# Performance work log

Hardware: AMD Instinct MI355X
Metric: run time of the kernel (lower is better)

The kernel has to match this reference:

```python
import jax, jax.numpy as jnp
import numpy as np

TEMPERATURE = 0.07
NEG_INF = -1e9


def setup_inputs() -> dict:
    key = jax.random.key(0)
    k1, k2, k3, k4, k5 = jax.random.split(key, 5)
    B, L, H = 64, 256, 64
    query_embs = jax.random.normal(k1, (B, L, H), dtype=jnp.float32)
    key_embs = jax.random.normal(k2, (B, L, H), dtype=jnp.float32)
    labels = jax.random.randint(k3, (B,), 0, 2, dtype=jnp.int64)
    q_mask = jax.random.randint(k4, (B, L), 0, 2, dtype=jnp.int32)
    k_mask = jax.random.randint(k5, (B, L), 0, 2, dtype=jnp.int32)
    return {"query_embs": query_embs, "key_embs": key_embs, "labels": labels,
            "q_mask": q_mask, "k_mask": k_mask}


def reference(query_embs, key_embs, labels, q_mask, k_mask):
    # ColBERT-style late interaction over all B x B pairs.
    # sim: (B_q, B_k, Lq, Lk) token-level dot products.
    sim = jnp.einsum('bqh,ckh->bcqk', query_embs, key_embs)
    # Mask out padded key tokens before the max over key positions.
    sim = jnp.where(k_mask[None, :, None, :].astype(bool), sim, NEG_INF)
    maxsim = jnp.max(sim, axis=-1)                      # (B_q, B_k, Lq)
    qm = q_mask[:, None, :].astype(maxsim.dtype)        # (B_q, 1, Lq)
    scores = jnp.sum(maxsim * qm, axis=-1) / TEMPERATURE  # (B_q, B_k)
    # Cross-entropy on rows with labels==1, target = diagonal index.
    logp = jax.nn.log_softmax(scores, axis=-1)
    B = scores.shape[0]
    diag = logp[jnp.arange(B), jnp.arange(B)]           # (B,)
    w = labels.astype(scores.dtype)
    denom = jnp.maximum(jnp.sum(w), 1.0)
    return -jnp.sum(w * diag) / denom
```

## Files before the change

### kernel.cpp

```cpp
#include <hip/hip_runtime.h>
#include <math.h>

#define PB 64
#define PL 256
#define PH 64
#define TEMP 0.07f
#define NEG_INF_F (-1e9f)

#define KFTILE 1024
#define KFSLAB (16 * KFTILE)
#define BGRP   2

typedef short short8 __attribute__((ext_vector_type(8)));
typedef float f32x4 __attribute__((ext_vector_type(4)));

__device__ __forceinline__ unsigned short f32_to_bf16(float f) {
    unsigned int u = __float_as_uint(f);
    u += 0x7FFFu + ((u >> 16) & 1u);
    return (unsigned short)(u >> 16);
}

__device__ __forceinline__ int frag_off(int p, int cc) {
    return ((p >> 4) * KFTILE) + ((cc >> 3) * 512) +
           (((((cc >> 1) & 3) * 16) + (p & 15)) * 8) + ((cc & 1) * 4);
}

__global__ __launch_bounds__(256)
void prep_kernel(const float* __restrict__ Q,
                 const float* __restrict__ K,
                 const int*   __restrict__ kmask,
                 const int*   __restrict__ qmask,
                 unsigned short* __restrict__ Qfrag,
                 unsigned short* __restrict__ Kfrag,
                 int* __restrict__ nvK,
                 int* __restrict__ nvQ) {
    const int tid  = threadIdx.x;
    const int lane = tid & 63;
    const int wave = tid >> 6;
    __shared__ int posArr[PL];
    __shared__ int wcnt[4];

    const bool isQ = (blockIdx.x >= 256);
    const int  bid = isQ ? (blockIdx.x - 256) : blockIdx.x;
    const int  idx     = bid >> 2;
    const int  quarter = bid & 3;

    const int* mask = isQ ? (qmask + idx * PL) : (kmask + idx * PL);
    const int km = mask[tid];
    unsigned long long bal = __ballot(km != 0);
    int within = __popcll(bal & ((1ull << lane) - 1ull));
    if (lane == 0) wcnt[wave] = __popcll(bal);
    __syncthreads();
    int base = 0;
    #pragma unroll
    for (int w = 0; w < 4; ++w) base += (w < wave) ? wcnt[w] : 0;
    posArr[tid] = km ? (base + within) : -1;
    const int nv = wcnt[0] + wcnt[1] + wcnt[2] + wcnt[3];
    __syncthreads();

    const int sub = lane >> 4;
    const int cl  = lane & 15;
    const float* src = (isQ ? Q : K) + (size_t)idx * PL * PH;
    unsigned short* slab = (isQ ? Qfrag : Kfrag) + (size_t)idx * KFSLAB;

    #pragma unroll
    for (int it = 0; it < 4; ++it) {
        int r = quarter * 64 + it * 16 + wave * 4 + sub;
        int p = posArr[r];
        if (p >= 0) {
            float4 v = *(const float4*)(src + (size_t)r * PH + cl * 4);
            ushort4 o;
            o.x = f32_to_bf16(v.x); o.y = f32_to_bf16(v.y);
            o.z = f32_to_bf16(v.z); o.w = f32_to_bf16(v.w);
            *(ushort4*)(slab + frag_off(p, cl)) = o;
        }
    }

    if (!isQ) {
        const int rows16 = (nv + 15) & ~15;
        const int padChunks = (rows16 - nv) * 16;
        if (tid < padChunks) {
            int row = nv + (tid >> 4);
            if (row >= quarter * 64 && row < quarter * 64 + 64)
                *(ushort4*)(slab + frag_off(row, tid & 15)) = (ushort4){0, 0, 0, 0};
        }
        if (quarter == 0 && tid == 0) nvK[idx] = nv;
    } else {
        #pragma unroll
        for (int it = 0; it < 4; ++it) {
            int id2 = it * 256 + tid;
            int row = quarter * 64 + (id2 >> 4);
            if (row >= nv)
                *(ushort4*)(slab + frag_off(row, id2 & 15)) = (ushort4){0, 0, 0, 0};
        }
        if (quarter == 0 && tid == 0) nvQ[idx] = nv;
    }
}

__global__ __launch_bounds__(256, 2)
void colbert_scores_mfma(const unsigned short* __restrict__ Qfrag,
                         const unsigned short* __restrict__ Kfrag,
                         const int*   __restrict__ nvK,
                         const int*   __restrict__ nvQ,
                         float*       __restrict__ scores) {
    const int c  = blockIdx.x;
    const int bg = blockIdx.y;
    const int tid  = threadIdx.x;
    const int wave = tid >> 6;
    const int lane = tid & 63;
    const int n    = lane & 15;

    __shared__ float red[BGRP][4];

    const int nv       = nvK[c];
    const int ntFull   = nv >> 4;
    const int tailCols = nv & 15;

    const int b0  = bg * BGRP;
    const int nq0 = nvQ[b0];
    const int nq1 = nvQ[b0 + 1];
    const int ntQP = ((nq0 > nq1 ? nq0 : nq1) + 31) >> 5;

    const f32x4 ZERO4 = (f32x4){0.f, 0.f, 0.f, 0.f};
    const float biasv = (n < tailCols) ? 0.0f : NEG_INF_F;
    const f32x4 BIAS4 = (f32x4){biasv, biasv, biasv, biasv};

    const unsigned short* kb = Kfrag + (size_t)c * KFSLAB + lane * 8;

    float partial[BGRP] = {0.0f, 0.0f};

    for (int qp = wave; qp < ntQP; qp += 4) {
        short8 aA[BGRP][2][2];
        #pragma unroll
        for (int bi = 0; bi < BGRP; ++bi) {
            const unsigned short* qbase = Qfrag + (size_t)(b0 + bi) * KFSLAB
                                         + qp * 2 * KFTILE + lane * 8;
            aA[bi][0][0] = *(const short8*)(qbase);
            aA[bi][0][1] = *(const short8*)(qbase + 512);
            aA[bi][1][0] = *(const short8*)(qbase + 1024);
            aA[bi][1][1] = *(const short8*)(qbase + 1536);
        }

        float maxv[BGRP][2][4];
        #pragma unroll
        for (int bi = 0; bi < BGRP; ++bi)
            #pragma unroll
            for (int t = 0; t < 2; ++t)
                #pragma unroll
                for (int r = 0; r < 4; ++r) maxv[bi][t][r] = NEG_INF_F;

        int ct = 0;
        for (; ct + 1 < ntFull; ct += 2) {
            const unsigned short* ka = kb + ct * KFTILE;
            short8 kA0 = *(const short8*)(ka);
            short8 kA1 = *(const short8*)(ka + 512);
            short8 kB0 = *(const short8*)(ka + 1024);
            short8 kB1 = *(const short8*)(ka + 1536);

            #pragma unroll
            for (int bi = 0; bi < BGRP; ++bi)
                #pragma unroll
                for (int t = 0; t < 2; ++t) {
                    f32x4 accA = __builtin_amdgcn_mfma_f32_16x16x32_bf16(aA[bi][t][0], kA0, ZERO4, 0, 0, 0);
                    accA = __builtin_amdgcn_mfma_f32_16x16x32_bf16(aA[bi][t][1], kA1, accA, 0, 0, 0);
                    f32x4 accB = __builtin_amdgcn_mfma_f32_16x16x32_bf16(aA[bi][t][0], kB0, ZERO4, 0, 0, 0);
                    accB = __builtin_amdgcn_mfma_f32_16x16x32_bf16(aA[bi][t][1], kB1, accB, 0, 0, 0);
                    #pragma unroll
                    for (int r = 0; r < 4; ++r)
                        maxv[bi][t][r] = fmaxf(maxv[bi][t][r], fmaxf(accA[r], accB[r]));
                }
        }

        if (ntFull & 1) {
            const unsigned short* ka = kb + ct * KFTILE;
            short8 k0 = *(const short8*)(ka);
            short8 k1 = *(const short8*)(ka + 512);
            #pragma unroll
            for (int bi = 0; bi < BGRP; ++bi)
                #pragma unroll
                for (int t = 0; t < 2; ++t) {
                    f32x4 acc = __builtin_amdgcn_mfma_f32_16x16x32_bf16(aA[bi][t][0], k0, ZERO4, 0, 0, 0);
                    acc = __builtin_amdgcn_mfma_f32_16x16x32_bf16(aA[bi][t][1], k1, acc, 0, 0, 0);
                    #pragma unroll
                    for (int r = 0; r < 4; ++r)
                        maxv[bi][t][r] = fmaxf(maxv[bi][t][r], acc[r]);
                }
            ct++;
        }

        if (tailCols) {
            const unsigned short* ka = kb + ct * KFTILE;
            short8 k0 = *(const short8*)(ka);
            short8 k1 = *(const short8*)(ka + 512);
            #pragma unroll
            for (int bi = 0; bi < BGRP; ++bi)
                #pragma unroll
                for (int t = 0; t < 2; ++t) {
                    f32x4 acc = __builtin_amdgcn_mfma_f32_16x16x32_bf16(aA[bi][t][0], k0, BIAS4, 0, 0, 0);
                    acc = __builtin_amdgcn_mfma_f32_16x16x32_bf16(aA[bi][t][1], k1, acc, 0, 0, 0);
                    #pragma unroll
                    for (int r = 0; r < 4; ++r)
                        maxv[bi][t][r] = fmaxf(maxv[bi][t][r], acc[r]);
                }
        }

        #pragma unroll
        for (int bi = 0; bi < BGRP; ++bi)
            #pragma unroll
            for (int t = 0; t < 2; ++t)
                #pragma unroll
                for (int r = 0; r < 4; ++r) {
                    float mv = maxv[bi][t][r];
                    mv = fmaxf(mv, __shfl_xor(mv, 1, 16));
                    mv = fmaxf(mv, __shfl_xor(mv, 2, 16));
                    mv = fmaxf(mv, __shfl_xor(mv, 4, 16));
                    mv = fmaxf(mv, __shfl_xor(mv, 8, 16));
                    if (n == 0) partial[bi] += mv;
                }
    }

    #pragma unroll
    for (int bi = 0; bi < BGRP; ++bi) {
        float p = partial[bi];
        p += __shfl_xor(p, 16, 64);
        p += __shfl_xor(p, 32, 64);
        if (lane == 0) red[bi][wave] = p;
    }

    __syncthreads();
    if (tid < BGRP) {
        float total = red[tid][0] + red[tid][1] + red[tid][2] + red[tid][3];
        scores[(b0 + tid) * PB + c] = total * (1.0f / TEMP);
    }
}

__global__ void finalize_kernel(const float* __restrict__ scores,
                                const int*   __restrict__ labels,
                                float*       __restrict__ out) {
    const int r = threadIdx.x;
    const float* row = scores + r * PB;
    float mx = NEG_INF_F;
    for (int j = 0; j < PB; ++j) mx = fmaxf(mx, row[j]);
    float se = 0.0f;
    for (int j = 0; j < PB; ++j) se += expf(row[j] - mx);
    float logp_diag = row[r] - mx - logf(se);
    float w = (float)labels[r];
    float wd = w * logp_diag;
    #pragma unroll
    for (int off = 32; off >= 1; off >>= 1) {
        wd += __shfl_xor(wd, off, 64);
        w  += __shfl_xor(w,  off, 64);
    }
    if (r == 0) out[0] = -wd / fmaxf(w, 1.0f);
}

extern "C" void kernel_launch(void* const* d_in, const int* in_sizes, int n_in,
                              void* d_out, int out_size, void* d_ws, size_t ws_size,
                              hipStream_t stream) {
    const float* Q      = (const float*)d_in[0];
    const float* K      = (const float*)d_in[1];
    const int*   labels = (const int*)d_in[2];
    const int*   qmask  = (const int*)d_in[3];
    const int*   kmask  = (const int*)d_in[4];
    float*       out    = (float*)d_out;

    char* ws = (char*)d_ws;
    float*          scores = (float*)ws;
    unsigned short* Qfrag  = (unsigned short*)(ws + 16 * 1024);
    unsigned short* Kfrag  = (unsigned short*)(ws + 16 * 1024 + 2 * 1024 * 1024);
    int*            nvK    = (int*)(ws + 16 * 1024 + 4 * 1024 * 1024);
    int*            nvQ    = nvK + 64;

    prep_kernel<<<512, 256, 0, stream>>>(Q, K, kmask, qmask, Qfrag, Kfrag, nvK, nvQ);

    dim3 grid(PB, PB / BGRP);
    colbert_scores_mfma<<<grid, 256, 0, stream>>>(Qfrag, Kfrag, nvK, nvQ, scores);
    finalize_kernel<<<1, 64, 0, stream>>>(scores, labels, out);
}
```

Baseline: 94.02 us.

## Keep key fragments in registers and assign whole query batches per wave

Each wave now loads all compacted key tiles for its key batch into registers once. It then loops over two query batches, each processed entirely by that wave, instead of having four waves split the query tiles of two batches. The block-level shared-memory reduction and barrier go away, and tail masking is folded into a per-tile bias. The aim is to cut repeated key loads and synchronisation, at the cost of much higher register pressure (a 16x2 short8 array), possible spills, and fewer blocks in the grid.

```diff
diff --git a/kernel.cpp b/kernel.cpp
--- a/kernel.cpp
+++ b/kernel.cpp
@@ -9,7 +9,7 @@
 
 #define KFTILE 1024
 #define KFSLAB (16 * KFTILE)
-#define BGRP   2
+#define BGRP   8
 
 typedef short short8 __attribute__((ext_vector_type(8)));
 typedef float f32x4 __attribute__((ext_vector_type(4)));
@@ -110,127 +110,79 @@
     const int lane = tid & 63;
     const int n    = lane & 15;
 
-    __shared__ float red[BGRP][4];
-
-    const int nv       = nvK[c];
-    const int ntFull   = nv >> 4;
-    const int tailCols = nv & 15;
-
-    const int b0  = bg * BGRP;
-    const int nq0 = nvQ[b0];
-    const int nq1 = nvQ[b0 + 1];
-    const int ntQP = ((nq0 > nq1 ? nq0 : nq1) + 31) >> 5;
+    const int nv   = nvK[c];
+    const int nt16 = (nv + 15) >> 4;
+
+    const unsigned short* kb = Kfrag + (size_t)c * KFSLAB + lane * 8;
+    short8 kreg[16][2];
+    #pragma unroll
+    for (int ct = 0; ct < 16; ++ct) {
+        if (ct < nt16) {
+            kreg[ct][0] = *(const short8*)(kb + ct * KFTILE);
+            kreg[ct][1] = *(const short8*)(kb + ct * KFTILE + 512);
+        }
+    }
 
     const f32x4 ZERO4 = (f32x4){0.f, 0.f, 0.f, 0.f};
-    const float biasv = (n < tailCols) ? 0.0f : NEG_INF_F;
-    const f32x4 BIAS4 = (f32x4){biasv, biasv, biasv, biasv};
-
-    const unsigned short* kb = Kfrag + (size_t)c * KFSLAB + lane * 8;
-
-    float partial[BGRP] = {0.0f, 0.0f};
-
-    for (int qp = wave; qp < ntQP; qp += 4) {
-        short8 aA[BGRP][2][2];
-        #pragma unroll
-        for (int bi = 0; bi < BGRP; ++bi) {
-            const unsigned short* qbase = Qfrag + (size_t)(b0 + bi) * KFSLAB
-                                         + qp * 2 * KFTILE + lane * 8;
-            aA[bi][0][0] = *(const short8*)(qbase);
-            aA[bi][0][1] = *(const short8*)(qbase + 512);
-            aA[bi][1][0] = *(const short8*)(qbase + 1024);
-            aA[bi][1][1] = *(const short8*)(qbase + 1536);
-        }
-
-        float maxv[BGRP][2][4];
-        #pragma unroll
-        for (int bi = 0; bi < BGRP; ++bi)
+
+    #pragma unroll 1
+    for (int bo = 0; bo < 2; ++bo) {
+        const int b  = bg * BGRP + wave * 2 + bo;
+        const int nq = nvQ[b];
+        const int nQP = (nq + 31) >> 5;
+        const unsigned short* qslab = Qfrag + (size_t)b * KFSLAB + lane * 8;
+
+        float partial = 0.0f;
+
+        #pragma unroll 1
+        for (int qp = 0; qp < nQP; ++qp) {
+            const unsigned short* qbase = qslab + qp * 2 * KFTILE;
+            short8 a00 = *(const short8*)(qbase);
+            short8 a01 = *(const short8*)(qbase + 512);
+            short8 a10 = *(const short8*)(qbase + 1024);
+            short8 a11 = *(const short8*)(qbase + 1536);
+
+            float maxv[2][4];
             #pragma unroll
             for (int t = 0; t < 2; ++t)
                 #pragma unroll
-                for (int r = 0; r < 4; ++r) maxv[bi][t][r] = NEG_INF_F;
-
-        int ct = 0;
-        for (; ct + 1 < ntFull; ct += 2) {
-            const unsigned short* ka = kb + ct * KFTILE;
-            short8 kA0 = *(const short8*)(ka);
-            short8 kA1 = *(const short8*)(ka + 512);
-            short8 kB0 = *(const short8*)(ka + 1024);
-            short8 kB1 = *(const short8*)(ka + 1536);
+                for (int r = 0; r < 4; ++r) maxv[t][r] = NEG_INF_F;
 
             #pragma unroll
-            for (int bi = 0; bi < BGRP; ++bi)
-                #pragma unroll
-                for (int t = 0; t < 2; ++t) {
-                    f32x4 accA = __builtin_amdgcn_mfma_f32_16x16x32_bf16(aA[bi][t][0], kA0, ZERO4, 0, 0, 0);
-                    accA = __builtin_amdgcn_mfma_f32_16x16x32_bf16(aA[bi][t][1], kA1, accA, 0, 0, 0);
-                    f32x4 accB = __builtin_amdgcn_mfma_f32_16x16x32_bf16(aA[bi][t][0], kB0, ZERO4, 0, 0, 0);
-                    accB = __builtin_amdgcn_mfma_f32_16x16x32_bf16(aA[bi][t][1], kB1, accB, 0, 0, 0);
+            for (int ct = 0; ct < 16; ++ct) {
+                if (ct < nt16) {
+                    const float bv = (ct * 16 + n < nv) ? 0.0f : NEG_INF_F;
+                    const f32x4 B4 = (f32x4){bv, bv, bv, bv};
+
+                    f32x4 acc0 = __builtin_amdgcn_mfma_f32_16x16x32_bf16(a00, kreg[ct][0], B4, 0, 0, 0);
+                    acc0 = __builtin_amdgcn_mfma_f32_16x16x32_bf16(a01, kreg[ct][1], acc0, 0, 0, 0);
+                    f32x4 acc1 = __builtin_amdgcn_mfma_f32_16x16x32_bf16(a10, kreg[ct][0], B4, 0, 0, 0);
+                    acc1 = __builtin_amdgcn_mfma_f32_16x16x32_bf16(a11, kreg[ct][1], acc1, 0, 0, 0);
+
                     #pragma unroll
-                    for (int r = 0; r < 4; ++r)
-                        maxv[bi][t][r] = fmaxf(maxv[bi][t][r], fmaxf(accA[r], accB[r]));
+                    for (int r = 0; r < 4; ++r) {
+                        maxv[0][r] = fmaxf(maxv[0][r], acc0[r]);
+                        maxv[1][r] = fmaxf(maxv[1][r], acc1[r]);
+                    }
                 }
-        }
-
-        if (ntFull & 1) {
-            const unsigned short* ka = kb + ct * KFTILE;
-            short8 k0 = *(const short8*)(ka);
-            short8 k1 = *(const short8*)(ka + 512);
-            #pragma unroll
-            for (int bi = 0; bi < BGRP; ++bi)
-                #pragma unroll
-                for (int t = 0; t < 2; ++t) {
-                    f32x4 acc = __builtin_amdgcn_mfma_f32_16x16x32_bf16(aA[bi][t][0], k0, ZERO4, 0, 0, 0);
-                    acc = __builtin_amdgcn_mfma_f32_16x16x32_bf16(aA[bi][t][1], k1, acc, 0, 0, 0);
-                    #pragma unroll
-                    for (int r = 0; r < 4; ++r)
-                        maxv[bi][t][r] = fmaxf(maxv[bi][t][r], acc[r]);
-                }
-            ct++;
-        }
-
-        if (tailCols) {
-            const unsigned short* ka = kb + ct * KFTILE;
-            short8 k0 = *(const short8*)(ka);
-            short8 k1 = *(const short8*)(ka + 512);
-            #pragma unroll
-            for (int bi = 0; bi < BGRP; ++bi)
-                #pragma unroll
-                for (int t = 0; t < 2; ++t) {
-                    f32x4 acc = __builtin_amdgcn_mfma_f32_16x16x32_bf16(aA[bi][t][0], k0, BIAS4, 0, 0, 0);
-                    acc = __builtin_amdgcn_mfma_f32_16x16x32_bf16(aA[bi][t][1], k1, acc, 0, 0, 0);
-                    #pragma unroll
-                    for (int r = 0; r < 4; ++r)
-                        maxv[bi][t][r] = fmaxf(maxv[bi][t][r], acc[r]);
-                }
-        }
-
-        #pragma unroll
-        for (int bi = 0; bi < BGRP; ++bi)
+            }
+
             #pragma unroll
             for (int t = 0; t < 2; ++t)
                 #pragma unroll
                 for (int r = 0; r < 4; ++r) {
-                    float mv = maxv[bi][t][r];
+                    float mv = maxv[t][r];
                     mv = fmaxf(mv, __shfl_xor(mv, 1, 16));
                     mv = fmaxf(mv, __shfl_xor(mv, 2, 16));
                     mv = fmaxf(mv, __shfl_xor(mv, 4, 16));
                     mv = fmaxf(mv, __shfl_xor(mv, 8, 16));
-                    if (n == 0) partial[bi] += mv;
+                    if (n == 0) partial += mv;
                 }
-    }
-
-    #pragma unroll
-    for (int bi = 0; bi < BGRP; ++bi) {
-        float p = partial[bi];
-        p += __shfl_xor(p, 16, 64);
-        p += __shfl_xor(p, 32, 64);
-        if (lane == 0) red[bi][wave] = p;
-    }
-
-    __syncthreads();
-    if (tid < BGRP) {
-        float total = red[tid][0] + red[tid][1] + red[tid][2] + red[tid][3];
-        scores[(b0 + tid) * PB + c] = total * (1.0f / TEMP);
+        }
+
+        partial += __shfl_xor(partial, 16, 64);
+        partial += __shfl_xor(partial, 32, 64);
+        if (lane == 0) scores[b * PB + c] = partial * (1.0f / TEMP);
     }
 }
 
```

New measurement: 98.84 us. +5.1%, slower.
